# Optimization experiments

Hardware: AMD Instinct MI355X
Metric: run time of the kernel (lower is better)

The kernel has to match this reference:

```python
import jax, jax.numpy as jnp
import numpy as np

N_NODES = 100000


def gcn_conv(x, W, b, src, dst, n):
    # PyG GCNConv: linear transform, add self-loops, symmetric deg^-1/2 norm,
    # scatter-sum messages from src -> dst, add bias.
    x = x @ W  # [N, out]
    loop = jnp.arange(n, dtype=src.dtype)
    src_sl = jnp.concatenate([src, loop])
    dst_sl = jnp.concatenate([dst, loop])
    deg = jax.ops.segment_sum(jnp.ones_like(dst_sl, dtype=x.dtype), dst_sl, num_segments=n)
    dinv = jax.lax.rsqrt(deg)
    norm = dinv[src_sl] * dinv[dst_sl]  # [E+N]
    msg = x[src_sl] * norm[:, None]
    out = jax.ops.segment_sum(msg, dst_sl, num_segments=n)
    return out + b


def base_gnn(x, edge_index, W1, b1, W2, b2):
    src, dst = edge_index[0], edge_index[1]
    n = x.shape[0]
    h = gcn_conv(x, W1, b1, src, dst, n)
    h = jax.nn.relu(h)
    return gcn_conv(h, W2, b2, src, dst, n)


def setup_inputs() -> dict:
    key = jax.random.key(0)
    ks = jax.random.split(key, 12)
    n, e, ep, en = N_NODES, 1600000, 200000, 200000
    in_ch, hid, out_ch, n_classes = 256, 128, 128, 10
    x = jax.random.normal(ks[0], (n, in_ch), dtype=jnp.float32)
    edge_index = jax.random.randint(ks[1], (2, e), 0, n, dtype=jnp.int64)
    edge_index_pos = jax.random.randint(ks[2], (2, ep), 0, n, dtype=jnp.int64)
    edge_index_neg = jax.random.randint(ks[3], (2, en), 0, n, dtype=jnp.int64)
    s1 = 1.0 / np.sqrt(in_ch)
    s2 = 1.0 / np.sqrt(hid)
    so = 1.0 / np.sqrt(out_ch)
    sl = 1.0 / np.sqrt(2 * out_ch)
    return {
        "x": x,
        "edge_index": edge_index,
        "edge_index_pos": edge_index_pos,
        "edge_index_neg": edge_index_neg,
        "W1": jax.random.uniform(ks[4], (in_ch, hid), jnp.float32, -s1, s1),
        "b1": jnp.zeros((hid,), jnp.float32),
        "W2": jax.random.uniform(ks[5], (hid, out_ch), jnp.float32, -s2, s2),
        "b2": jnp.zeros((out_ch,), jnp.float32),
        "Wcls": jax.random.uniform(ks[6], (out_ch, n_classes), jnp.float32, -so, so),
        "bcls": jax.random.uniform(ks[7], (n_classes,), jnp.float32, -so, so),
        "Wlink": jax.random.uniform(ks[8], (2 * out_ch, 1), jnp.float32, -sl, sl),
        "blink": jax.random.uniform(ks[9], (1,), jnp.float32, -sl, sl),
    }


def reference(x, edge_index, edge_index_pos, edge_index_neg,
              W1, b1, W2, b2, Wcls, bcls, Wlink, blink):
    # Shared base embedding (math identical to torch's redundant recompute)
    h = base_gnn(x, edge_index, W1, b1, W2, b2)  # [N, 128]
    # Node head
    node_logits = jax.nn.relu(h) @ Wcls + bcls
    node_pred = jax.nn.log_softmax(node_logits, axis=1)
    # Link head: gather endpoint embeddings, concat, linear
    xp = jnp.concatenate([h[edge_index_pos[0]], h[edge_index_pos[1]]], axis=1)
    xn = jnp.concatenate([h[edge_index_neg[0]], h[edge_index_neg[1]]], axis=1)
    link_pos = (xp @ Wlink + blink)[:, 0]
    link_neg = (xn @ Wlink + blink)[:, 0]
    return (node_pred, link_pos, link_neg)
```

## Files before the change

### kernel.cpp

```cpp
#include <hip/hip_runtime.h>
#include <stdint.h>

typedef __attribute__((ext_vector_type(8))) short bf16x8;
typedef __attribute__((ext_vector_type(4))) float f32x4;

__device__ __forceinline__ float b2f(uint32_t h) {
    union { uint32_t u; float f; } v; v.u = h << 16; return v.f;
}
__device__ __forceinline__ ushort f2b(float f) {
    union { float f; uint32_t u; } v; v.f = f;
    uint32_t u = v.u;
    return (ushort)((u + 0x7fffu + ((u >> 16) & 1u)) >> 16);
}
__device__ __forceinline__ float ldin(const void* p, int i, int fp32) {
    return fp32 ? ((const float*)p)[i] : b2f(((const ushort*)p)[i]);
}
__device__ __forceinline__ bf16x8 pack8(float4 a, float4 b) {
    bf16x8 r;
    r[0] = (short)f2b(a.x); r[1] = (short)f2b(a.y);
    r[2] = (short)f2b(a.z); r[3] = (short)f2b(a.w);
    r[4] = (short)f2b(b.x); r[5] = (short)f2b(b.y);
    r[6] = (short)f2b(b.z); r[7] = (short)f2b(b.w);
    return r;
}

__global__ void k_flags(const void* W1, const void* ei, int* flags) {
    int l = threadIdx.x;
    const ushort* w = (const ushort*)W1;
    float a0 = fabsf(b2f(w[l]));
    float a1 = fabsf(b2f(w[64 + l]));
    bool bad = !(a0 <= 0.25f) || !(a1 <= 0.25f);
    unsigned long long mb = __ballot(bad);
    const int* e = (const int*)ei;
    bool z = (l < 16) ? (e[2 * l + 1] == 0) : false;
    unsigned long long mz = __ballot(z);
    if (l == 0) {
        flags[0] = mb ? 1 : 0;
        flags[1] = (__popcll(mz & 0xffffull) >= 15) ? 1 : 0;
    }
}

__global__ __launch_bounds__(256) void k_cvt_idx(const void* ei, const void* ep, const void* en,
                                                 int* cEi, int* cEp, int* cEn,
                                                 int twoE, int twoEp, int twoEn, int N,
                                                 const int* __restrict__ flags) {
    int i = blockIdx.x * 256 + threadIdx.x;
    int i64 = flags[1];
    const void* srcp; int* dstp; int j = i;
    if (i < twoE) { srcp = ei; dstp = cEi; }
    else if (i < twoE + twoEp) { srcp = ep; dstp = cEp; j = i - twoE; }
    else if (i < twoE + twoEp + twoEn) { srcp = en; dstp = cEn; j = i - twoE - twoEp; }
    else return;
    int v = i64 ? (int)((const long long*)srcp)[j] : ((const int*)srcp)[j];
    v = v < 0 ? 0 : (v >= N ? N - 1 : v);
    dstp[j] = v;
}

__global__ __launch_bounds__(256) void k_cvt_w(const void* W1, const void* W2, const void* Wc,
                                               const void* b1, const void* b2, const void* bc,
                                               const void* Wl, const void* bl,
                                               ushort* Wt1, ushort* Wt2, ushort* WtC,
                                               ushort* b1c, ushort* b2c, ushort* bcc,
                                               ushort* Wlc, ushort* blc,
                                               const int* __restrict__ flags) {
    int i = blockIdx.x * 256 + threadIdx.x;
    int f = flags[0];
    if (i < 32768) {
        int c = i >> 8, k = i & 255;
        Wt1[i] = f2b(ldin(W1, k * 128 + c, f));
    } else if (i < 49152) {
        int j = i - 32768, c = j >> 7, k = j & 127;
        Wt2[j] = f2b(ldin(W2, k * 128 + c, f));
    } else if (i < 51200) {
        int j = i - 49152, c = j >> 7, k = j & 127;
        ushort v = 0;
        if (c < 10) v = f2b(ldin(Wc, k * 10 + c, f));
        WtC[j] = v;
    } else if (i < 51328) {
        int j = i - 51200; b1c[j] = f2b(ldin(b1, j, f));
    } else if (i < 51456) {
        int j = i - 51328; b2c[j] = f2b(ldin(b2, j, f));
    } else if (i < 51472) {
        int j = i - 51456;
        ushort v = 0;
        if (j < 10) v = f2b(ldin(bc, j, f));
        bcc[j] = v;
    } else if (i < 51728) {
        int j = i - 51472; Wlc[j] = f2b(ldin(Wl, j, f));
    } else if (i < 51736) {
        int j = i - 51728;
        ushort v = 0;
        if (j < 1) v = f2b(ldin(bl, 0, f));
        blc[j] = v;
    }
}

__global__ __launch_bounds__(256) void k_hist1(const int* __restrict__ dst, int* __restrict__ histM,
                                               int E, int NB1) {
    __shared__ int h[512];
    for (int j = threadIdx.x; j < 512; j += 256) h[j] = 0;
    __syncthreads();
    int base = blockIdx.x * 4096;
    for (int j = threadIdx.x; j < 4096; j += 256) {
        int i = base + j;
        if (i < E) atomicAdd(&h[dst[i] >> 8], 1);
    }
    __syncthreads();
    for (int j = threadIdx.x; j < 512; j += 256)
        histM[j * NB1 + blockIdx.x] = h[j];
}

__global__ __launch_bounds__(1024) void k_mscan_block(const int* __restrict__ in, int* __restrict__ out,
                                                      int* __restrict__ bsum, int len) {
    __shared__ int sh[1024];
    int t = threadIdx.x;
    int i = blockIdx.x * 1024 + t;
    int val = (i < len) ? in[i] : 0;
    sh[t] = val; __syncthreads();
    for (int off = 1; off < 1024; off <<= 1) {
        int v = (t >= off) ? sh[t - off] : 0;
        __syncthreads();
        sh[t] += v;
        __syncthreads();
    }
    if (i < len) out[i] = sh[t] - val;
    if (t == 1023) bsum[blockIdx.x] = sh[1023];
}

__global__ __launch_bounds__(1024) void k_mscan_top(int* __restrict__ bsum, int nb) {
    __shared__ int sh[1024];
    int t = threadIdx.x;
    int val = (t < nb) ? bsum[t] : 0;
    sh[t] = val; __syncthreads();
    for (int off = 1; off < 1024; off <<= 1) {
        int v = (t >= off) ? sh[t - off] : 0;
        __syncthreads();
        sh[t] += v;
        __syncthreads();
    }
    if (t < nb) bsum[t] = sh[t] - val;
}

__global__ __launch_bounds__(1024) void k_mscan_add(int* __restrict__ out, const int* __restrict__ bsum, int len) {
    int i = blockIdx.x * 1024 + threadIdx.x;
    if (i < len) out[i] += bsum[blockIdx.x];
}

__global__ __launch_bounds__(512) void k_cbs(const int* __restrict__ off, int* __restrict__ cbs, int E, int NB1) {
    int t = threadIdx.x;
    cbs[t] = off[t * NB1];
    if (t == 0) cbs[512] = E;
}

__global__ __launch_bounds__(256) void k_scatter1(const int* __restrict__ src, const int* __restrict__ dst,
                                                  const int* __restrict__ off, int2* __restrict__ grouped,
                                                  int E, int NB1) {
    __shared__ int o[512];
    for (int j = threadIdx.x; j < 512; j += 256) o[j] = off[j * NB1 + blockIdx.x];
    __syncthreads();
    int base = blockIdx.x * 4096;
    for (int j = threadIdx.x; j < 4096; j += 256) {
        int i = base + j;
        if (i < E) {
            int d = dst[i];
            int p = atomicAdd(&o[d >> 8], 1);
            grouped[p] = make_int2(src[i], d);
        }
    }
}

__global__ __launch_bounds__(256) void k_deg2(const int2* __restrict__ grouped, const int* __restrict__ cbs,
                                              int* __restrict__ deg, int N) {
    __shared__ int c[256];
    c[threadIdx.x] = 0;
    __syncthreads();
    int b = blockIdx.x;
    int s0 = cbs[b], s1 = cbs[b + 1];
    for (int i = s0 + threadIdx.x; i < s1; i += 256)
        atomicAdd(&c[grouped[i].y & 255], 1);
    __syncthreads();
    int v = b * 256 + threadIdx.x;
    if (v < N) deg[v] = c[threadIdx.x];
}

__global__ __launch_bounds__(1024) void k_scan_block(const int* __restrict__ deg, int* __restrict__ rowptr,
                                                     float* __restrict__ dinv, int* __restrict__ bsum, int n) {
    __shared__ int sh[1024];
    int t = threadIdx.x;
    int i = blockIdx.x * 1024 + t;
    int val = (i < n) ? deg[i] : 0;
    sh[t] = val; __syncthreads();
    for (int off = 1; off < 1024; off <<= 1) {
        int v = (t >= off) ? sh[t - off] : 0;
        __syncthreads();
        sh[t] += v;
        __syncthreads();
    }
    if (i < n) {
        rowptr[i] = sh[t] - val;
        dinv[i] = rsqrtf((float)(val + 1));
    }
    if (t == 1023) bsum[blockIdx.x] = sh[1023];
}

__global__ __launch_bounds__(128) void k_scan_top(const int* __restrict__ bsum, int* __restrict__ boff, int nb) {
    __shared__ int sh[128];
    int t = threadIdx.x;
    int val = (t < nb) ? bsum[t] : 0;
    sh[t] = val; __syncthreads();
    for (int off = 1; off < 128; off <<= 1) {
        int v = (t >= off) ? sh[t - off] : 0;
        __syncthreads();
        sh[t] += v;
        __syncthreads();
    }
    if (t < nb) boff[t] = sh[t] - val;
}

__global__ __launch_bounds__(1024) void k_scan_add(int* __restrict__ rowptr, const int* __restrict__ boff,
                                                   int n, int E) {
    int i = blockIdx.x * 1024 + threadIdx.x;
    if (i < n) rowptr[i] += boff[blockIdx.x];
    if (i == 0) rowptr[n] = E;
}

__global__ __launch_bounds__(256) void k_fill2(const int2* __restrict__ grouped, const int* __restrict__ cbs,
                                               const int* __restrict__ rowptr, const float* __restrict__ dinv,
                                               int2* __restrict__ edge, int N) {
    __shared__ int o[256];
    int b = blockIdx.x;
    int v = b * 256 + threadIdx.x;
    o[threadIdx.x] = (v < N) ? rowptr[v] : 0;
    __syncthreads();
    int s0 = cbs[b], s1 = cbs[b + 1];
    for (int i = s0 + threadIdx.x; i < s1; i += 256) {
        int2 e = grouped[i];
        int p = atomicAdd(&o[e.y & 255], 1);
        float w = dinv[e.x] * dinv[e.y];
        edge[p] = make_int2(e.x, __float_as_int(w));
    }
}

template <int K, bool SEL>
__global__ __launch_bounds__(256, 2) void k_gemm(const void* __restrict__ Xraw,
                                                 const int* __restrict__ flags,
                                                 const ushort* __restrict__ Wt,
                                                 ushort* __restrict__ Out, int nrows) {
    constexpr int NS = K / 32;
    __shared__ uint4 sB[NS * 8 * 64];

    const int tid = threadIdx.x;
    for (int it = tid; it < NS * 8 * 64; it += 256) {
        int l = it & 63, fn = it >> 6;
        int s = fn >> 3, n = fn & 7;
        int mr = l & 15, q = l >> 4;
        sB[it] = *(const uint4*)(Wt + (size_t)(n * 16 + mr) * K + s * 32 + q * 8);
    }
    __syncthreads();

    const bool f32in = SEL && flags[0];
    const int wave = tid >> 6;
    const int l = tid & 63;
    const int q = l >> 4, mr = l & 15;
    const int gw = blockIdx.x * 4 + wave;
    const int nw = gridDim.x * 4;
    const int ntile = (nrows + 15) >> 4;

    for (int tp = gw; tp * 2 < ntile; tp += nw) {
        const int t0 = tp * 2;
        const bool has1 = (t0 + 1 < ntile);
        const int t1 = has1 ? t0 + 1 : t0;
        const int r0 = min(t0 * 16 + mr, nrows - 1);
        const int r1 = min(t1 * 16 + mr, nrows - 1);

        bf16x8 a0[NS], a1[NS];
        if (f32in) {
            const float* x0 = (const float*)Xraw + (size_t)r0 * K + q * 8;
            const float* x1 = (const float*)Xraw + (size_t)r1 * K + q * 8;
#pragma unroll
            for (int s = 0; s < NS; ++s) {
                float4 a = *(const float4*)(x0 + s * 32);
                float4 b = *(const float4*)(x0 + s * 32 + 4);
                a0[s] = pack8(a, b);
            }
#pragma unroll
            for (int s = 0; s < NS; ++s) {
                float4 a = *(const float4*)(x1 + s * 32);
                float4 b = *(const float4*)(x1 + s * 32 + 4);
                a1[s] = pack8(a, b);
            }
        } else {
            const ushort* x0 = (const ushort*)Xraw + (size_t)r0 * K + q * 8;
            const ushort* x1 = (const ushort*)Xraw + (size_t)r1 * K + q * 8;
#pragma unroll
            for (int s = 0; s < NS; ++s) a0[s] = *(const bf16x8*)(x0 + s * 32);
#pragma unroll
            for (int s = 0; s < NS; ++s) a1[s] = *(const bf16x8*)(x1 + s * 32);
        }

        f32x4 acc0[8], acc1[8];
#pragma unroll
        for (int n = 0; n < 8; ++n) {
            acc0[n] = (f32x4){0.f, 0.f, 0.f, 0.f};
            acc1[n] = (f32x4){0.f, 0.f, 0.f, 0.f};
        }
#pragma unroll
        for (int s = 0; s < NS; ++s) {
#pragma unroll
            for (int n = 0; n < 8; ++n) {
                bf16x8 b = __builtin_bit_cast(bf16x8, sB[(s * 8 + n) * 64 + l]);
                acc0[n] = __builtin_amdgcn_mfma_f32_16x16x32_bf16(a0[s], b, acc0[n], 0, 0, 0);
                acc1[n] = __builtin_amdgcn_mfma_f32_16x16x32_bf16(a1[s], b, acc1[n], 0, 0, 0);
            }
        }
#pragma unroll
        for (int n = 0; n < 8; ++n) {
#pragma unroll
            for (int r = 0; r < 4; ++r) {
                int row0 = t0 * 16 + q * 4 + r;
                if (row0 < nrows) Out[(size_t)row0 * 128 + n * 16 + mr] = f2b(acc0[n][r]);
                if (has1) {
                    int row1 = t1 * 16 + q * 4 + r;
                    if (row1 < nrows) Out[(size_t)row1 * 128 + n * 16 + mr] = f2b(acc1[n][r]);
                }
            }
        }
    }
}

__device__ __forceinline__ void fma8(float* acc, uint4 p, float w) {
    uint32_t pu[4] = {p.x, p.y, p.z, p.w};
#pragma unroll
    for (int k = 0; k < 4; ++k) {
        float lo = __uint_as_float(pu[k] << 16);
        float hi = __uint_as_float(pu[k] & 0xffff0000u);
        acc[2 * k]     += lo * w;
        acc[2 * k + 1] += hi * w;
    }
}

__global__ __launch_bounds__(256) void k_conv(const ushort* __restrict__ XW, const int* __restrict__ rowptr,
                                              const int2* __restrict__ edge, const float* __restrict__ dinv,
                                              const ushort* __restrict__ bias, ushort* __restrict__ Hout,
                                              int n, int relu) {
    int wave = threadIdx.x >> 6;
    int v = blockIdx.x * 4 + wave;
    if (v >= n) return;
    int l = threadIdx.x & 63;
    int g = l >> 4;
    int c = l & 15;

    int s0 = rowptr[v], s1 = rowptr[v + 1];
    float dv = dinv[v];
    float wself = (g == 0) ? dv * dv : 0.f;

    uint4 pv = *(const uint4*)(XW + (size_t)v * 128 + c * 8);
    float acc[8];
    {
        uint32_t pu[4] = {pv.x, pv.y, pv.z, pv.w};
#pragma unroll
        for (int k = 0; k < 4; ++k) {
            acc[2 * k]     = __uint_as_float(pu[k] << 16) * wself;
            acc[2 * k + 1] = __uint_as_float(pu[k] & 0xffff0000u) * wself;
        }
    }

    int i = s0;
    while (i + 8 <= s1) {
        int2 eA = edge[i + g];
        int2 eB = edge[i + 4 + g];
        uint4 pA = *(const uint4*)(XW + (size_t)eA.x * 128 + c * 8);
        uint4 pB = *(const uint4*)(XW + (size_t)eB.x * 128 + c * 8);
        fma8(acc, pA, __int_as_float(eA.y));
        fma8(acc, pB, __int_as_float(eB.y));
        i += 8;
    }
    if (i + 4 <= s1) {
        int2 e = edge[i + g];
        uint4 p = *(const uint4*)(XW + (size_t)e.x * 128 + c * 8);
        fma8(acc, p, __int_as_float(e.y));
        i += 4;
    }
    if (i < s1) {
        int ei = i + g;
        bool val = ei < s1;
        int2 e = edge[val ? ei : s0];
        uint4 p = *(const uint4*)(XW + (size_t)e.x * 128 + c * 8);
        fma8(acc, p, val ? __int_as_float(e.y) : 0.f);
    }

#pragma unroll
    for (int k = 0; k < 8; ++k) {
        acc[k] += __shfl_xor(acc[k], 16);
        acc[k] += __shfl_xor(acc[k], 32);
    }

    if (g == 0) {
        uint4 bb = *(const uint4*)(bias + c * 8);
        uint32_t bu[4] = {bb.x, bb.y, bb.z, bb.w};
        uint4 o;
        uint32_t* op = (uint32_t*)&o;
#pragma unroll
        for (int k = 0; k < 4; ++k) {
            float lo = acc[2 * k]     + __uint_as_float(bu[k] << 16);
            float hi = acc[2 * k + 1] + __uint_as_float(bu[k] & 0xffff0000u);
            if (relu) { lo = fmaxf(lo, 0.f); hi = fmaxf(hi, 0.f); }
            op[k] = (uint32_t)f2b(lo) | ((uint32_t)f2b(hi) << 16);
        }
        *(uint4*)(Hout + (size_t)v * 128 + c * 8) = o;
    }
}

__global__ __launch_bounds__(256) void k_nodehead(const ushort* __restrict__ H, const ushort* __restrict__ WtC,
                                                  const ushort* __restrict__ bcc, void* __restrict__ out,
                                                  int n, const int* __restrict__ flags) {
    int wave = threadIdx.x >> 6;
    int gw = blockIdx.x * 4 + wave;
    if (gw * 16 >= n) return;
    int fp32o = flags[0];
    int l = threadIdx.x & 63;
    int q = l >> 4, mr = l & 15;
    int m0 = gw * 16;

    f32x4 acc = (f32x4){0.f, 0.f, 0.f, 0.f};
    const ushort* hrow = H + (size_t)(m0 + mr) * 128 + q * 8;
#pragma unroll
    for (int s = 0; s < 4; ++s) {
        bf16x8 a = *(const bf16x8*)(hrow + s * 32);
#pragma unroll
        for (int j = 0; j < 8; ++j) {
            ushort t = (ushort)a[j];
            if (t & 0x8000u) a[j] = 0;
        }
        bf16x8 b = *(const bf16x8*)(WtC + (size_t)mr * 128 + s * 32 + q * 8);
        acc = __builtin_amdgcn_mfma_f32_16x16x32_bf16(a, b, acc, 0, 0, 0);
    }

    float bc = b2f(bcc[mr]);
#pragma unroll
    for (int r = 0; r < 4; ++r) {
        float logit = acc[r] + bc;
        float m = (mr < 10) ? logit : -1e30f;
#pragma unroll
        for (int off = 1; off < 16; off <<= 1) m = fmaxf(m, __shfl_xor(m, off, 16));
        float ex = (mr < 10) ? expf(logit - m) : 0.f;
        float ssum = ex;
#pragma unroll
        for (int off = 1; off < 16; off <<= 1) ssum += __shfl_xor(ssum, off, 16);
        if (mr < 10) {
            float lsm = logit - m - logf(ssum);
            size_t idx = (size_t)(m0 + q * 4 + r) * 10 + mr;
            if (fp32o) ((float*)out)[idx] = lsm;
            else ((ushort*)out)[idx] = f2b(lsm);
        }
    }
}

__global__ __launch_bounds__(256) void k_link(const ushort* __restrict__ H, const int* __restrict__ pos,
                                              const int* __restrict__ neg, const ushort* __restrict__ Wlc,
                                              const ushort* __restrict__ blc, void* __restrict__ out,
                                              size_t obase, int Ep, int En, const int* __restrict__ flags) {
    int wave = threadIdx.x >> 6;
    int l = threadIdx.x & 63;
    int g = l >> 4, t = l & 15;
    int e = (blockIdx.x * 4 + wave) * 4 + g;
    if (e >= Ep + En) return;
    int fp32o = flags[0];

    const int* P; int eb, off2;
    if (e < Ep) { P = pos; eb = e; off2 = Ep; }
    else { P = neg; eb = e - Ep; off2 = En; }
    int sI = P[eb], dI = P[off2 + eb];

    bf16x8 hs = *(const bf16x8*)(H + (size_t)sI * 128 + t * 8);
    bf16x8 hd = *(const bf16x8*)(H + (size_t)dI * 128 + t * 8);
    bf16x8 w0 = *(const bf16x8*)(Wlc + t * 8);
    bf16x8 w1 = *(const bf16x8*)(Wlc + 128 + t * 8);

    float acc = 0.f;
#pragma unroll
    for (int j = 0; j < 8; ++j) {
        acc += b2f((ushort)hs[j]) * b2f((ushort)w0[j]);
        acc += b2f((ushort)hd[j]) * b2f((ushort)w1[j]);
    }
#pragma unroll
    for (int off = 1; off < 16; off <<= 1) acc += __shfl_xor(acc, off, 16);
    if (t == 0) {
        float vf = acc + b2f(blc[0]);
        size_t idx = obase + (size_t)e;
        if (fp32o) ((float*)out)[idx] = vf;
        else ((ushort*)out)[idx] = f2b(vf);
    }
}

extern "C" void kernel_launch(void* const* d_in, const int* in_sizes, int n_in,
                              void* d_out, int out_size, void* d_ws, size_t ws_size,
                              hipStream_t stream) {
    const void* x    = d_in[0];
    const void* ei   = d_in[1];
    const void* eip  = d_in[2];
    const void* ein  = d_in[3];
    const void* W1   = d_in[4];
    const void* b1   = d_in[5];
    const void* W2   = d_in[6];
    const void* b2   = d_in[7];
    const void* Wcls = d_in[8];
    const void* bcls = d_in[9];
    const void* Wl   = d_in[10];
    const void* bl   = d_in[11];

    const int N  = in_sizes[0] / 256;
    const int E  = in_sizes[1] / 2;
    const int Ep = in_sizes[2] / 2;
    const int En = in_sizes[3] / 2;

    const int NB1  = (E + 4095) / 4096;
    const int mlen = 512 * NB1;
    const int mb   = (mlen + 1023) / 1024;

    char* ws = (char*)d_ws;
    size_t off = 0;
    auto alloc = [&](size_t bytes) -> void* {
        void* p = ws + off;
        off = (off + bytes + 255) & ~(size_t)255;
        return p;
    };
    int*    flags  = (int*)alloc(256);
    ushort* bufXW  = (ushort*)alloc((size_t)N * 128 * 2);
    ushort* bufH   = (ushort*)alloc((size_t)N * 128 * 2);
    int*    cEi    = (int*)alloc((size_t)2 * E * 4);
    int*    cEp    = (int*)alloc((size_t)2 * Ep * 4);
    int*    cEn    = (int*)alloc((size_t)2 * En * 4);
    int2*   grouped= (int2*)alloc((size_t)E * 8);
    int*    histM  = (int*)alloc((size_t)mlen * 4);
    int*    offM   = (int*)alloc((size_t)mlen * 4);
    int*    msum   = (int*)alloc(4096);
    int*    cbs    = (int*)alloc(513 * 4);
    float*  dinv   = (float*)alloc((size_t)N * 4);
    int*    deg    = (int*)alloc((size_t)N * 4);
    int*    rowp   = (int*)alloc((size_t)(N + 1) * 4);
    int2*   edge   = (int2*)alloc((size_t)E * 8);
    int*    bsum   = (int*)alloc(1024);
    int*    boff   = (int*)alloc(1024);
    ushort* Wt1    = (ushort*)alloc(65536);
    ushort* Wt2    = (ushort*)alloc(32768);
    ushort* WtC    = (ushort*)alloc(4096);
    ushort* b1c    = (ushort*)alloc(256);
    ushort* b2c    = (ushort*)alloc(256);
    ushort* bcc    = (ushort*)alloc(64);
    ushort* Wlc    = (ushort*)alloc(512);
    ushort* blc    = (ushort*)alloc(64);

    k_flags<<<1, 64, 0, stream>>>(W1, ei, flags);

    int twoE = 2 * E, twoEp = 2 * Ep, twoEn = 2 * En;
    int idx_total = twoE + twoEp + twoEn;
    k_cvt_idx<<<(idx_total + 255) / 256, 256, 0, stream>>>(ei, eip, ein, cEi, cEp, cEn,
                                                           twoE, twoEp, twoEn, N, flags);
    k_cvt_w<<<203, 256, 0, stream>>>(W1, W2, Wcls, b1, b2, bcls, Wl, bl,
                                     Wt1, Wt2, WtC, b1c, b2c, bcc, Wlc, blc, flags);

    const int* srcp = cEi;
    const int* dstp = cEi + E;

    k_hist1<<<NB1, 256, 0, stream>>>(dstp, histM, E, NB1);
    k_mscan_block<<<mb, 1024, 0, stream>>>(histM, offM, msum, mlen);
    k_mscan_top<<<1, 1024, 0, stream>>>(msum, mb);
    k_mscan_add<<<mb, 1024, 0, stream>>>(offM, msum, mlen);
    k_cbs<<<1, 512, 0, stream>>>(offM, cbs, E, NB1);
    k_scatter1<<<NB1, 256, 0, stream>>>(srcp, dstp, offM, grouped, E, NB1);
    k_deg2<<<512, 256, 0, stream>>>(grouped, cbs, deg, N);
    int nb = (N + 1023) / 1024;
    k_scan_block<<<nb, 1024, 0, stream>>>(deg, rowp, dinv, bsum, N);
    k_scan_top<<<1, 128, 0, stream>>>(bsum, boff, nb);
    k_scan_add<<<nb, 1024, 0, stream>>>(rowp, boff, N, E);
    k_fill2<<<512, 256, 0, stream>>>(grouped, cbs, rowp, dinv, edge, N);

    k_gemm<256, true><<<512, 256, 0, stream>>>(x, flags, Wt1, bufXW, N);
    k_conv<<<(N + 3) / 4, 256, 0, stream>>>(bufXW, rowp, edge, dinv, b1c, bufH, N, 1);
    k_gemm<128, false><<<768, 256, 0, stream>>>(bufH, flags, Wt2, bufXW, N);
    k_conv<<<(N + 3) / 4, 256, 0, stream>>>(bufXW, rowp, edge, dinv, b2c, bufH, N, 0);

    int head_blocks = ((N + 15) / 16 + 3) / 4;
    k_nodehead<<<head_blocks, 256, 0, stream>>>(bufH, WtC, bcc, d_out, N, flags);
    k_link<<<(Ep + En + 3) / 4, 256, 0, stream>>>(bufH, cEp, cEn, Wlc, blc, d_out,
                                                  (size_t)N * 10, Ep, En, flags);
}
```

Before: 525.0 us.

## Pre-swizzle GEMM inputs into MFMA fragment layout and vectorize output stores

A new conversion kernel rewrites the input features into bf16 laid out in MFMA fragment order. The first conv kernel also writes its output in that tiled layout, so both GEMMs can load their A operands as contiguous coalesced 16-byte chunks. The MFMA operands are swapped so each lane holds four consecutive output columns of one row, which lets the stores be packed 8-byte writes instead of scattered 2-byte writes. The cost is an extra kernel launch and a full read and write of x into a workspace buffer.

```diff
diff --git a/kernel.cpp b/kernel.cpp
--- a/kernel.cpp
+++ b/kernel.cpp
@@ -14,14 +14,6 @@
 }
 __device__ __forceinline__ float ldin(const void* p, int i, int fp32) {
     return fp32 ? ((const float*)p)[i] : b2f(((const ushort*)p)[i]);
-}
-__device__ __forceinline__ bf16x8 pack8(float4 a, float4 b) {
-    bf16x8 r;
-    r[0] = (short)f2b(a.x); r[1] = (short)f2b(a.y);
-    r[2] = (short)f2b(a.z); r[3] = (short)f2b(a.w);
-    r[4] = (short)f2b(b.x); r[5] = (short)f2b(b.y);
-    r[6] = (short)f2b(b.z); r[7] = (short)f2b(b.w);
-    return r;
 }
 
 __global__ void k_flags(const void* W1, const void* ei, int* flags) {
@@ -95,6 +87,30 @@
     }
 }
 
+__global__ __launch_bounds__(256) void k_cvt_x(const void* __restrict__ x, ushort* __restrict__ xc,
+                                               int N, const int* __restrict__ flags) {
+    int gw = blockIdx.x * 4 + (threadIdx.x >> 6);
+    int ntile = (N + 15) >> 4;
+    if (gw >= ntile * 8) return;
+    int tile = gw >> 3, s = gw & 7;
+    int l = threadIdx.x & 63, mr = l & 15, q = l >> 4;
+    int row = tile * 16 + mr;
+    if (row > N - 1) row = N - 1;
+    uint4 o;
+    if (flags[0]) {
+        const float* xf = (const float*)x + (size_t)row * 256 + s * 32 + q * 8;
+        float4 a = *(const float4*)xf;
+        float4 b = *(const float4*)(xf + 4);
+        o.x = (uint32_t)f2b(a.x) | ((uint32_t)f2b(a.y) << 16);
+        o.y = (uint32_t)f2b(a.z) | ((uint32_t)f2b(a.w) << 16);
+        o.z = (uint32_t)f2b(b.x) | ((uint32_t)f2b(b.y) << 16);
+        o.w = (uint32_t)f2b(b.z) | ((uint32_t)f2b(b.w) << 16);
+    } else {
+        o = *(const uint4*)((const ushort*)x + (size_t)row * 256 + s * 32 + q * 8);
+    }
+    *(uint4*)(xc + ((size_t)gw * 64 + l) * 8) = o;
+}
+
 __global__ __launch_bounds__(256) void k_hist1(const int* __restrict__ dst, int* __restrict__ histM,
                                                int E, int NB1) {
     __shared__ int h[512];
@@ -241,12 +257,10 @@
     }
 }
 
-template <int K, bool SEL>
-__global__ __launch_bounds__(256, 2) void k_gemm(const void* __restrict__ Xraw,
-                                                 const int* __restrict__ flags,
+template <int NS>
+__global__ __launch_bounds__(256, 2) void k_gemm(const ushort* __restrict__ Xf,
                                                  const ushort* __restrict__ Wt,
                                                  ushort* __restrict__ Out, int nrows) {
-    constexpr int NS = K / 32;
     __shared__ uint4 sB[NS * 8 * 64];
 
     const int tid = threadIdx.x;
@@ -254,11 +268,10 @@
         int l = it & 63, fn = it >> 6;
         int s = fn >> 3, n = fn & 7;
         int mr = l & 15, q = l >> 4;
-        sB[it] = *(const uint4*)(Wt + (size_t)(n * 16 + mr) * K + s * 32 + q * 8);
+        sB[it] = *(const uint4*)(Wt + (size_t)(n * 16 + mr) * (NS * 32) + s * 32 + q * 8);
     }
     __syncthreads();
 
-    const bool f32in = SEL && flags[0];
     const int wave = tid >> 6;
     const int l = tid & 63;
     const int q = l >> 4, mr = l & 15;
@@ -270,33 +283,14 @@
         const int t0 = tp * 2;
         const bool has1 = (t0 + 1 < ntile);
         const int t1 = has1 ? t0 + 1 : t0;
-        const int r0 = min(t0 * 16 + mr, nrows - 1);
-        const int r1 = min(t1 * 16 + mr, nrows - 1);
 
         bf16x8 a0[NS], a1[NS];
-        if (f32in) {
-            const float* x0 = (const float*)Xraw + (size_t)r0 * K + q * 8;
-            const float* x1 = (const float*)Xraw + (size_t)r1 * K + q * 8;
-#pragma unroll
-            for (int s = 0; s < NS; ++s) {
-                float4 a = *(const float4*)(x0 + s * 32);
-                float4 b = *(const float4*)(x0 + s * 32 + 4);
-                a0[s] = pack8(a, b);
-            }
-#pragma unroll
-            for (int s = 0; s < NS; ++s) {
-                float4 a = *(const float4*)(x1 + s * 32);
-                float4 b = *(const float4*)(x1 + s * 32 + 4);
-                a1[s] = pack8(a, b);
-            }
-        } else {
-            const ushort* x0 = (const ushort*)Xraw + (size_t)r0 * K + q * 8;
-            const ushort* x1 = (const ushort*)Xraw + (size_t)r1 * K + q * 8;
-#pragma unroll
-            for (int s = 0; s < NS; ++s) a0[s] = *(const bf16x8*)(x0 + s * 32);
-#pragma unroll
-            for (int s = 0; s < NS; ++s) a1[s] = *(const bf16x8*)(x1 + s * 32);
-        }
+        const ushort* x0 = Xf + ((size_t)t0 * NS * 64 + l) * 8;
+        const ushort* x1 = Xf + ((size_t)t1 * NS * 64 + l) * 8;
+#pragma unroll
+        for (int s = 0; s < NS; ++s) a0[s] = *(const bf16x8*)(x0 + s * 512);
+#pragma unroll
+        for (int s = 0; s < NS; ++s) a1[s] = *(const bf16x8*)(x1 + s * 512);
 
         f32x4 acc0[8], acc1[8];
 #pragma unroll
@@ -309,19 +303,31 @@
 #pragma unroll
             for (int n = 0; n < 8; ++n) {
                 bf16x8 b = __builtin_bit_cast(bf16x8, sB[(s * 8 + n) * 64 + l]);
-                acc0[n] = __builtin_amdgcn_mfma_f32_16x16x32_bf16(a0[s], b, acc0[n], 0, 0, 0);
-                acc1[n] = __builtin_amdgcn_mfma_f32_16x16x32_bf16(a1[s], b, acc1[n], 0, 0, 0);
+                acc0[n] = __builtin_amdgcn_mfma_f32_16x16x32_bf16(b, a0[s], acc0[n], 0, 0, 0);
+                acc1[n] = __builtin_amdgcn_mfma_f32_16x16x32_bf16(b, a1[s], acc1[n], 0, 0, 0);
             }
         }
-#pragma unroll
-        for (int n = 0; n < 8; ++n) {
-#pragma unroll
-            for (int r = 0; r < 4; ++r) {
-                int row0 = t0 * 16 + q * 4 + r;
-                if (row0 < nrows) Out[(size_t)row0 * 128 + n * 16 + mr] = f2b(acc0[n][r]);
-                if (has1) {
-                    int row1 = t1 * 16 + q * 4 + r;
-                    if (row1 < nrows) Out[(size_t)row1 * 128 + n * 16 + mr] = f2b(acc1[n][r]);
+        int row0 = t0 * 16 + mr;
+        if (row0 < nrows) {
+            ushort* orow = Out + (size_t)row0 * 128 + q * 4;
+#pragma unroll
+            for (int n = 0; n < 8; ++n) {
+                uint2 o;
+                o.x = (uint32_t)f2b(acc0[n][0]) | ((uint32_t)f2b(acc0[n][1]) << 16);
+                o.y = (uint32_t)f2b(acc0[n][2]) | ((uint32_t)f2b(acc0[n][3]) << 16);
+                *(uint2*)(orow + n * 16) = o;
+            }
+        }
+        if (has1) {
+            int row1 = t1 * 16 + mr;
+            if (row1 < nrows) {
+                ushort* orow = Out + (size_t)row1 * 128 + q * 4;
+#pragma unroll
+                for (int n = 0; n < 8; ++n) {
+                    uint2 o;
+                    o.x = (uint32_t)f2b(acc1[n][0]) | ((uint32_t)f2b(acc1[n][1]) << 16);
+                    o.y = (uint32_t)f2b(acc1[n][2]) | ((uint32_t)f2b(acc1[n][3]) << 16);
+                    *(uint2*)(orow + n * 16) = o;
                 }
             }
         }
@@ -342,7 +348,7 @@
 __global__ __launch_bounds__(256) void k_conv(const ushort* __restrict__ XW, const int* __restrict__ rowptr,
                                               const int2* __restrict__ edge, const float* __restrict__ dinv,
                                               const ushort* __restrict__ bias, ushort* __restrict__ Hout,
-                                              int n, int relu) {
+                                              int n, int relu, int frag) {
     int wave = threadIdx.x >> 6;
     int v = blockIdx.x * 4 + wave;
     if (v >= n) return;
@@ -407,7 +413,13 @@
             if (relu) { lo = fmaxf(lo, 0.f); hi = fmaxf(hi, 0.f); }
             op[k] = (uint32_t)f2b(lo) | ((uint32_t)f2b(hi) << 16);
         }
-        *(uint4*)(Hout + (size_t)v * 128 + c * 8) = o;
+        if (frag) {
+            int tile = v >> 4, mr = v & 15;
+            size_t chunk = ((size_t)(tile * 4 + (c >> 2)) * 64 + (c & 3) * 16 + mr);
+            *(uint4*)(Hout + chunk * 8) = o;
+        } else {
+            *(uint4*)(Hout + (size_t)v * 128 + c * 8) = o;
+        }
     }
 }
 
@@ -517,6 +529,7 @@
     const int NB1  = (E + 4095) / 4096;
     const int mlen = 512 * NB1;
     const int mb   = (mlen + 1023) / 1024;
+    const int ntile = (N + 15) / 16;
 
     char* ws = (char*)d_ws;
     size_t off = 0;
@@ -526,8 +539,9 @@
         return p;
     };
     int*    flags  = (int*)alloc(256);
+    ushort* xc     = (ushort*)alloc((size_t)ntile * 8 * 64 * 16);
     ushort* bufXW  = (ushort*)alloc((size_t)N * 128 * 2);
-    ushort* bufH   = (ushort*)alloc((size_t)N * 128 * 2);
+    ushort* bufH   = (ushort*)alloc((size_t)ntile * 4 * 64 * 16);
     int*    cEi    = (int*)alloc((size_t)2 * E * 4);
     int*    cEp    = (int*)alloc((size_t)2 * Ep * 4);
     int*    cEn    = (int*)alloc((size_t)2 * En * 4);
@@ -559,6 +573,7 @@
                                                            twoE, twoEp, twoEn, N, flags);
     k_cvt_w<<<203, 256, 0, stream>>>(W1, W2, Wcls, b1, b2, bcls, Wl, bl,
                                      Wt1, Wt2, WtC, b1c, b2c, bcc, Wlc, blc, flags);
+    k_cvt_x<<<(ntile * 8 + 3) / 4, 256, 0, stream>>>(x, xc, N, flags);
 
     const int* srcp = cEi;
     const int* dstp = cEi + E;
@@ -576,10 +591,10 @@
     k_scan_add<<<nb, 1024, 0, stream>>>(rowp, boff, N, E);
     k_fill2<<<512, 256, 0, stream>>>(grouped, cbs, rowp, dinv, edge, N);
 
-    k_gemm<256, true><<<512, 256, 0, stream>>>(x, flags, Wt1, bufXW, N);
-    k_conv<<<(N + 3) / 4, 256, 0, stream>>>(bufXW, rowp, edge, dinv, b1c, bufH, N, 1);
-    k_gemm<128, false><<<768, 256, 0, stream>>>(bufH, flags, Wt2, bufXW, N);
-    k_conv<<<(N + 3) / 4, 256, 0, stream>>>(bufXW, rowp, edge, dinv, b2c, bufH, N, 0);
+    k_gemm<8><<<512, 256, 0, stream>>>(xc, Wt1, bufXW, N);
+    k_conv<<<(N + 3) / 4, 256, 0, stream>>>(bufXW, rowp, edge, dinv, b1c, bufH, N, 1, 1);
+    k_gemm<4><<<768, 256, 0, stream>>>(bufH, Wt2, bufXW, N);
+    k_conv<<<(N + 3) / 4, 256, 0, stream>>>(bufXW, rowp, edge, dinv, b2c, bufH, N, 0, 0);
 
     int head_blocks = ((N + 15) / 16 + 3) / 4;
     k_nodehead<<<head_blocks, 256, 0, stream>>>(bufH, WtC, bcc, d_out, N, flags);
```

Result: no change. 526.9 us (+0.3%).
